# Performance work log

Hardware: AMD Instinct MI355X
Metric: run time of the kernel (lower is better)

## Reference

```python
import jax, jax.numpy as jnp
import numpy as np

B, L, S, D, H, DH = 32, 96, 96, 512, 8, 64  # d_ff = S*S = 9216


def setup_inputs() -> dict:
    key = jax.random.key(0)
    ks = jax.random.split(key, 13)
    sc = 0.02
    inp = {
        "queries": jax.random.normal(ks[0], (B, L, D), jnp.float32),
        "keys": jax.random.normal(ks[1], (B, S, D), jnp.float32),
        "values": jax.random.normal(ks[2], (B, S, D), jnp.float32),
        "attn_mask": jnp.zeros((B, L, S), dtype=bool),
        # projections stored as (in, out); torch Linear is x @ W.T + b
        "Wq": jax.random.normal(ks[3], (D, H * DH), jnp.float32) * sc,
        "bq": jnp.zeros((H * DH,), jnp.float32),
        "Wk": jax.random.normal(ks[4], (D, H * DH), jnp.float32) * sc,
        "bk": jnp.zeros((H * DH,), jnp.float32),
        "Wv": jax.random.normal(ks[5], (D, H * DH), jnp.float32) * sc,
        "bv": jnp.zeros((H * DH,), jnp.float32),
        # core_value initialized as softmax over rank dim, as in the module
        "core": jax.nn.softmax(jax.random.normal(ks[6], (H, DH), jnp.float32), axis=-1),
        "Wo": jax.random.normal(ks[7], (S * S, D), jnp.float32) * sc,
        "bo": jnp.zeros((D,), jnp.float32),
    }
    return inp


def reference(queries, keys, values, attn_mask, Wq, bq, Wk, bk, Wv, bv, core, Wo, bo):
    b, l, _ = queries.shape
    s = keys.shape[1]
    h, d = core.shape
    # NOTE: the original uses .view(H, B, L, -1) on a (B, L, H*d) tensor —
    # a raw reshape, NOT a transpose. Replicate faithfully.
    q = (queries @ Wq + bq).reshape(h, b, l, d)
    k = (keys @ Wk + bk).reshape(h, b, s, d)
    v = (values @ Wv + bv).reshape(h, b, s, d)
    # per-head rank-d CP contraction, summed over heads, averaged by 1/H
    full = jnp.einsum("nh,nbih,nbjh,nbkh->bijk", core, q, k, v) / h  # [B,L,S,S]
    full = full.reshape(b, l, s * s)
    out = full @ Wo + bo  # [B, L, D]
    return out
```

## Files before the change

kernel.cpp:

```cpp
#include <hip/hip_runtime.h>
#include <hip/hip_bf16.h>
#include <stdint.h>

using bf16 = __hip_bfloat16;
typedef float v4f __attribute__((ext_vector_type(4)));
typedef short short8 __attribute__((ext_vector_type(8)));


__device__ __forceinline__ void async_cp16(void* l, const void* g) {
  __builtin_amdgcn_global_load_lds(
      (const __attribute__((address_space(1))) void*)(uintptr_t)g,
      (__attribute__((address_space(3))) void*)(uintptr_t)l, 16, 0, 0);
}

__global__ __launch_bounds__(256) void prep(
    const float* __restrict__ Wo, const float* __restrict__ Wq,
    const float* __restrict__ Wk, const float* __restrict__ Wv,
    const float* __restrict__ Xq, const float* __restrict__ Xk,
    const float* __restrict__ Xv, const float* __restrict__ bo,
    bf16* __restrict__ WoT, bf16* __restrict__ WTq,
    bf16* __restrict__ WTk, bf16* __restrict__ WTv,
    bf16* __restrict__ Xbq, bf16* __restrict__ Xbk, bf16* __restrict__ Xbv,
    float* __restrict__ out) {
  const int bid = blockIdx.x, t = threadIdx.x;
  if (bid < 5376) {
    __shared__ bf16 T[32][33];
    const float* src; bf16* dst; int K, N, kx, ny;
    if (bid < 4608) {
      src = Wo; dst = WoT; K = 9216; N = 512; kx = bid % 288; ny = bid / 288;
    } else {
      const int r = bid - 4608, which = r >> 8, rr = r & 255;
      kx = rr & 15; ny = rr >> 4; K = 512; N = 512;
      src = which == 0 ? Wq : (which == 1 ? Wk : Wv);
      dst = which == 0 ? WTq : (which == 1 ? WTk : WTv);
    }
    const int k0 = kx * 32, n0 = ny * 32;
    const int r = t >> 3, c = (t & 7) * 4;
    float4 v = *reinterpret_cast<const float4*>(src + (size_t)(k0 + r) * N + n0 + c);
    T[c + 0][r] = __float2bfloat16(v.x);
    T[c + 1][r] = __float2bfloat16(v.y);
    T[c + 2][r] = __float2bfloat16(v.z);
    T[c + 3][r] = __float2bfloat16(v.w);
    __syncthreads();
    union { uint2 u; bf16 h[4]; } o;
    o.h[0] = T[r][c + 0]; o.h[1] = T[r][c + 1];
    o.h[2] = T[r][c + 2]; o.h[3] = T[r][c + 3];
    *reinterpret_cast<uint2*>(dst + (size_t)(n0 + r) * K + k0 + c) = o.u;
  } else if (bid < 6528) {
    const int r = bid - 5376;
    const int which = r / 384, blk = r % 384;
    const float* src = which == 0 ? Xq : (which == 1 ? Xk : Xv);
    bf16* dst = which == 0 ? Xbq : (which == 1 ? Xbk : Xbv);
    const int base = blk * 4096 + t * 16;
    float4 a = *reinterpret_cast<const float4*>(src + base);
    float4 b = *reinterpret_cast<const float4*>(src + base + 4);
    float4 c = *reinterpret_cast<const float4*>(src + base + 8);
    float4 d = *reinterpret_cast<const float4*>(src + base + 12);
    union { uint4 u; bf16 h[8]; } o1, o2;
    o1.h[0] = __float2bfloat16(a.x); o1.h[1] = __float2bfloat16(a.y);
    o1.h[2] = __float2bfloat16(a.z); o1.h[3] = __float2bfloat16(a.w);
    o1.h[4] = __float2bfloat16(b.x); o1.h[5] = __float2bfloat16(b.y);
    o1.h[6] = __float2bfloat16(b.z); o1.h[7] = __float2bfloat16(b.w);
    o2.h[0] = __float2bfloat16(c.x); o2.h[1] = __float2bfloat16(c.y);
    o2.h[2] = __float2bfloat16(c.z); o2.h[3] = __float2bfloat16(c.w);
    o2.h[4] = __float2bfloat16(d.x); o2.h[5] = __float2bfloat16(d.y);
    o2.h[6] = __float2bfloat16(d.z); o2.h[7] = __float2bfloat16(d.w);
    *reinterpret_cast<uint4*>(dst + base) = o1.u;
    *reinterpret_cast<uint4*>(dst + base + 8) = o2.u;
  } else {
    const int r = bid - 6528;
    const int idx = (r * 256 + t) * 4;
    *reinterpret_cast<float4*>(out + idx) =
        *reinterpret_cast<const float4*>(bo + (idx & 511));
  }
}

__global__ __launch_bounds__(256) void proj_mfma(
    const bf16* __restrict__ Xb0, const bf16* __restrict__ Xb1,
    const bf16* __restrict__ Xb2,
    const bf16* __restrict__ WT0, const bf16* __restrict__ WT1,
    const bf16* __restrict__ WT2,
    const float* __restrict__ b0, const float* __restrict__ b1,
    const float* __restrict__ b2, const float* __restrict__ core,
    bf16* __restrict__ O0, bf16* __restrict__ O1, bf16* __restrict__ O2) {
  const int z = blockIdx.z;
  const bf16* X    = z == 0 ? Xb0 : (z == 1 ? Xb1 : Xb2);
  const bf16* WT   = z == 0 ? WT0 : (z == 1 ? WT1 : WT2);
  const float* bia = z == 0 ? b0 : (z == 1 ? b1 : b2);
  bf16* O          = z == 0 ? O0 : (z == 1 ? O1 : O2);

  const int bm = blockIdx.x * 128, bn = blockIdx.y * 64;
  __shared__ __align__(16) bf16 As[128 * 128];
  __shared__ __align__(16) bf16 Bs[64 * 128];
  const int t = threadIdx.x;
  const int w = t >> 6, lane = t & 63;
  const int m16 = lane & 15, q = lane >> 4;
  const int l16 = lane >> 4, l15 = lane & 15;

  v4f acc[2][4] = {};

  for (int k0 = 0; k0 < 512; k0 += 128) {
    __syncthreads();
    #pragma unroll
    for (int c = 0; c < 8; c++) {
      const int row = (w * 8 + c) * 4 + l16;
      const int lch = l15 ^ (row & 7);
      async_cp16(&As[(w * 8 + c) * 512],
                 X + (size_t)(bm + row) * 512 + k0 + lch * 8);
    }
    #pragma unroll
    for (int c = 0; c < 4; c++) {
      const int row = (w * 4 + c) * 4 + l16;
      const int lch = l15 ^ (row & 7);
      async_cp16(&Bs[(w * 4 + c) * 512],
                 WT + (size_t)(bn + row) * 512 + k0 + lch * 8);
    }
    __syncthreads();

    #pragma unroll
    for (int s = 0; s < 4; s++) {
      const int pc = ((s * 4 + q) ^ (m16 & 7)) * 8;
      short8 af[2], bfr[4];
      #pragma unroll
      for (int mt = 0; mt < 2; mt++)
        af[mt] = *reinterpret_cast<const short8*>(
            &As[(w * 32 + mt * 16 + m16) * 128 + pc]);
      #pragma unroll
      for (int nt = 0; nt < 4; nt++)
        bfr[nt] = *reinterpret_cast<const short8*>(
            &Bs[(nt * 16 + m16) * 128 + pc]);
      #pragma unroll
      for (int mt = 0; mt < 2; mt++)
        #pragma unroll
        for (int nt = 0; nt < 4; nt++)
          acc[mt][nt] = __builtin_amdgcn_mfma_f32_16x16x32_bf16(
              af[mt], bfr[nt], acc[mt][nt], 0, 0, 0);
    }
  }

  const bool isQ = (z == 0);
  const int nblk = bm / 384;
  #pragma unroll
  for (int mt = 0; mt < 2; mt++)
    #pragma unroll
    for (int nt = 0; nt < 4; nt++)
      #pragma unroll
      for (int r = 0; r < 4; r++) {
        const int row = bm + w * 32 + mt * 16 + q * 4 + r;
        const int col = bn + nt * 16 + m16;
        float v = acc[mt][nt][r] + bia[col];
        if (isQ) v *= core[nblk * 64 + (col & 63)] * 0.125f;
        O[(size_t)row * 512 + col] = __float2bfloat16(v);
      }
}

__global__ __launch_bounds__(256) void stage_b_mfma(
    const bf16* __restrict__ AQ, const bf16* __restrict__ KPb,
    const bf16* __restrict__ VPb, bf16* __restrict__ FULL) {
  const int b = blockIdx.y;
  const int i0 = blockIdx.x * 2;

  __shared__ __align__(16) bf16 smem[19456];
  bf16* Ks0 = smem;
  bf16* Ks1 = smem + 6144;
  bf16* Vs  = smem + 12288;
  bf16* aqs = smem + 18432;

  const int t = threadIdx.x;
  const int w = t >> 6, lane = t & 63;
  const int wr = w >> 1, wc = w & 1;
  const int m16 = lane & 15, q = lane >> 4;
  const int l8 = lane >> 3, l7 = lane & 7;

  if (t < 128) {
    const int isel = t & 1, n = t >> 4, seg = (t >> 1) & 7;
    *reinterpret_cast<uint4*>(&aqs[isel * 512 + n * 64 + seg * 8]) =
        *reinterpret_cast<const uint4*>(
            AQ + (size_t)n * 196608 + b * 6144 + (i0 + isel) * 64 + seg * 8);
  }

  union U8 { uint4 u; bf16 h[8]; };
  const int colq = (t & 7) * 8;
  const int rowk = t >> 3;
  const int krow7 = rowk & 7;

  U8 kk[3];
  {
    const bf16* Kp = KPb + b * 6144;
    #pragma unroll
    for (int c3 = 0; c3 < 3; c3++)
      kk[c3].u = *reinterpret_cast<const uint4*>(Kp + (t + c3 * 256) * 8);
  }

  v4f acc[2][3][3] = {};

  for (int n = 0; n < 8; n++) {
    __syncthreads();
    const bf16* Vp = VPb + (size_t)n * 196608 + b * 6144;
    #pragma unroll
    for (int c = 0; c < 3; c++) {
      const int r0 = (w * 3 + c) * 8;
      async_cp16(&Vs[(w * 3 + c) * 512],
                 Vp + (r0 + l8) * 64 + (l7 ^ l8) * 8);
    }
    float a0f[8], a1f[8];
    {
      U8 a0, a1;
      a0.u = *reinterpret_cast<const uint4*>(&aqs[n * 64 + colq]);
      a1.u = *reinterpret_cast<const uint4*>(&aqs[512 + n * 64 + colq]);
      #pragma unroll
      for (int e = 0; e < 8; e++) {
        a0f[e] = __bfloat162float(a0.h[e]);
        a1f[e] = __bfloat162float(a1.h[e]);
      }
    }
    #pragma unroll
    for (int c3 = 0; c3 < 3; c3++) {
      U8 s0, s1;
      #pragma unroll
      for (int e = 0; e < 8; e++) {
        const float kv = __bfloat162float(kk[c3].h[e]);
        s0.h[e] = __float2bfloat16(kv * a0f[e]);
        s1.h[e] = __float2bfloat16(kv * a1f[e]);
      }
      const int phys = (rowk + 32 * c3) * 64 + (l7 ^ krow7) * 8;
      *reinterpret_cast<uint4*>(&Ks0[phys]) = s0.u;
      *reinterpret_cast<uint4*>(&Ks1[phys]) = s1.u;
    }
    __syncthreads();
    if (n < 7) {
      const bf16* Kp1 = KPb + (size_t)(n + 1) * 196608 + b * 6144;
      #pragma unroll
      for (int c3 = 0; c3 < 3; c3++)
        kk[c3].u = *reinterpret_cast<const uint4*>(Kp1 + (t + c3 * 256) * 8);
    }

    #pragma unroll
    for (int s = 0; s < 2; s++) {
      const int pc = ((s * 4 + q) ^ (m16 & 7)) * 8;
      short8 bfr[3], af0[3], af1[3];
      #pragma unroll
      for (int cc = 0; cc < 3; cc++)
        bfr[cc] = *reinterpret_cast<const short8*>(
            &Vs[(wc * 48 + cc * 16 + m16) * 64 + pc]);
      #pragma unroll
      for (int a = 0; a < 3; a++) {
        af0[a] = *reinterpret_cast<const short8*>(
            &Ks0[(wr * 48 + a * 16 + m16) * 64 + pc]);
        af1[a] = *reinterpret_cast<const short8*>(
            &Ks1[(wr * 48 + a * 16 + m16) * 64 + pc]);
      }
      #pragma unroll
      for (int a = 0; a < 3; a++)
        #pragma unroll
        for (int cc = 0; cc < 3; cc++) {
          acc[0][a][cc] = __builtin_amdgcn_mfma_f32_16x16x32_bf16(
              af0[a], bfr[cc], acc[0][a][cc], 0, 0, 0);
          acc[1][a][cc] = __builtin_amdgcn_mfma_f32_16x16x32_bf16(
              af1[a], bfr[cc], acc[1][a][cc], 0, 0, 0);
        }
    }
  }

  __syncthreads();
  #pragma unroll
  for (int isel = 0; isel < 2; isel++)
    #pragma unroll
    for (int a = 0; a < 3; a++)
      #pragma unroll
      for (int cc = 0; cc < 3; cc++) {
        const int j0 = wr * 48 + a * 16, k0c = wc * 48 + cc * 16;
        #pragma unroll
        for (int r = 0; r < 4; r++)
          smem[isel * 9216 + (j0 + q * 4 + r) * 96 + k0c + m16] =
              __float2bfloat16(acc[isel][a][cc][r]);
      }
  __syncthreads();
  const size_t obase = (size_t)(b * 96 + i0) * 9216;
  #pragma unroll
  for (int c = t; c < 2304; c += 256)
    *reinterpret_cast<uint4*>(FULL + obase + c * 8) =
        *reinterpret_cast<const uint4*>(&smem[c * 8]);
}

__global__ __launch_bounds__(256) void stage_c_mfma(
    const bf16* __restrict__ FULL, const bf16* __restrict__ WoT,
    float* __restrict__ out) {
  const int bm = blockIdx.x * 128, bn = blockIdx.y * 64;
  const int kbase = blockIdx.z * 2304;
  __shared__ __align__(16) bf16 As[128 * 128];
  __shared__ __align__(16) bf16 Bs[64 * 128];
  const int t = threadIdx.x;
  const int w = t >> 6, lane = t & 63;
  const int m16 = lane & 15, q = lane >> 4;
  const int l16 = lane >> 4, l15 = lane & 15;

  v4f acc[2][4] = {};

  for (int k0 = kbase; k0 < kbase + 2304; k0 += 128) {
    __syncthreads();
    #pragma unroll
    for (int c = 0; c < 8; c++) {
      const int row = (w * 8 + c) * 4 + l16;
      const int lch = l15 ^ (row & 7);
      async_cp16(&As[(w * 8 + c) * 512],
                 FULL + (size_t)(bm + row) * 9216 + k0 + lch * 8);
    }
    #pragma unroll
    for (int c = 0; c < 4; c++) {
      const int row = (w * 4 + c) * 4 + l16;
      const int lch = l15 ^ (row & 7);
      async_cp16(&Bs[(w * 4 + c) * 512],
                 WoT + (size_t)(bn + row) * 9216 + k0 + lch * 8);
    }
    __syncthreads();

    #pragma unroll
    for (int s = 0; s < 4; s++) {
      const int pc = ((s * 4 + q) ^ (m16 & 7)) * 8;
      short8 af[2], bfr[4];
      #pragma unroll
      for (int mt = 0; mt < 2; mt++)
        af[mt] = *reinterpret_cast<const short8*>(
            &As[(w * 32 + mt * 16 + m16) * 128 + pc]);
      #pragma unroll
      for (int nt = 0; nt < 4; nt++)
        bfr[nt] = *reinterpret_cast<const short8*>(
            &Bs[(nt * 16 + m16) * 128 + pc]);
      #pragma unroll
      for (int mt = 0; mt < 2; mt++)
        #pragma unroll
        for (int nt = 0; nt < 4; nt++)
          acc[mt][nt] = __builtin_amdgcn_mfma_f32_16x16x32_bf16(
              af[mt], bfr[nt], acc[mt][nt], 0, 0, 0);
    }
  }

  #pragma unroll
  for (int mt = 0; mt < 2; mt++)
    #pragma unroll
    for (int nt = 0; nt < 4; nt++)
      #pragma unroll
      for (int r = 0; r < 4; r++) {
        const int row = bm + w * 32 + mt * 16 + q * 4 + r;
        const int col = bn + nt * 16 + m16;
        atomicAdd(&out[(size_t)row * 512 + col], acc[mt][nt][r]);
      }
}

extern "C" void kernel_launch(void* const* d_in, const int* in_sizes, int n_in,
                              void* d_out, int out_size, void* d_ws, size_t ws_size,
                              hipStream_t stream) {
  const float* queries = (const float*)d_in[0];
  const float* keys    = (const float*)d_in[1];
  const float* values  = (const float*)d_in[2];
  const float* Wq   = (const float*)d_in[4];
  const float* bq   = (const float*)d_in[5];
  const float* Wk   = (const float*)d_in[6];
  const float* bk   = (const float*)d_in[7];
  const float* Wv   = (const float*)d_in[8];
  const float* bv   = (const float*)d_in[9];
  const float* core = (const float*)d_in[10];
  const float* Wo   = (const float*)d_in[11];
  const float* bo   = (const float*)d_in[12];
  float* out = (float*)d_out;

  char* ws = (char*)d_ws;
  bf16* AQb = (bf16*)(ws);
  bf16* KPb = (bf16*)(ws + 3145728);
  bf16* VPb = (bf16*)(ws + 6291456);
  bf16* WTq = (bf16*)(ws + 9437184);
  bf16* WTk = (bf16*)(ws + 9961472);
  bf16* WTv = (bf16*)(ws + 10485760);
  bf16* WoT = (bf16*)(ws + 11010048);
  bf16* FULL = (bf16*)(ws + 20447232);
  bf16* Xbq = FULL;
  bf16* Xbk = FULL + 1572864;
  bf16* Xbv = FULL + 3145728;

  const dim3 blk(256);

  prep<<<dim3(8064), blk, 0, stream>>>(
      Wo, Wq, Wk, Wv, queries, keys, values, bo,
      WoT, WTq, WTk, WTv, Xbq, Xbk, Xbv, out);

  proj_mfma<<<dim3(24, 8, 3), blk, 0, stream>>>(
      Xbq, Xbk, Xbv, WTq, WTk, WTv, bq, bk, bv, core, AQb, KPb, VPb);

  stage_b_mfma<<<dim3(48, 32), blk, 0, stream>>>(AQb, KPb, VPb, FULL);

  stage_c_mfma<<<dim3(24, 8, 4), blk, 0, stream>>>(FULL, WoT, out);
}
```

Baseline: 205.4 us.

## Load A operand directly from global and halve tile rows in proj and stage_c GEMMs

Both the projection GEMM and the final Wo GEMM stop staging the A operand in LDS. Each wave now loads its A fragments straight from global memory, while B is still staged through swizzled LDS. Blocks shrink to 128 threads with 64-row tiles and the grids double to cover the same work. This is meant to cut LDS usage and barrier cost and raise occupancy, but it risks uncoalesced strided global loads for A, since each lane reads 16 bytes from a different row.

Result: slower. 236.6 us (+15.2%).

```diff
diff --git a/kernel.cpp b/kernel.cpp
--- a/kernel.cpp
+++ b/kernel.cpp
@@ -75,7 +75,7 @@
   }
 }
 
-__global__ __launch_bounds__(256) void proj_mfma(
+__global__ __launch_bounds__(128) void proj_mfma(
     const bf16* __restrict__ Xb0, const bf16* __restrict__ Xb1,
     const bf16* __restrict__ Xb2,
     const bf16* __restrict__ WT0, const bf16* __restrict__ WT1,
@@ -89,8 +89,7 @@
   const float* bia = z == 0 ? b0 : (z == 1 ? b1 : b2);
   bf16* O          = z == 0 ? O0 : (z == 1 ? O1 : O2);
 
-  const int bm = blockIdx.x * 128, bn = blockIdx.y * 64;
-  __shared__ __align__(16) bf16 As[128 * 128];
+  const int bm = blockIdx.x * 64, bn = blockIdx.y * 64;
   __shared__ __align__(16) bf16 Bs[64 * 128];
   const int t = threadIdx.x;
   const int w = t >> 6, lane = t & 63;
@@ -105,26 +104,20 @@
     for (int c = 0; c < 8; c++) {
       const int row = (w * 8 + c) * 4 + l16;
       const int lch = l15 ^ (row & 7);
-      async_cp16(&As[(w * 8 + c) * 512],
-                 X + (size_t)(bm + row) * 512 + k0 + lch * 8);
-    }
-    #pragma unroll
-    for (int c = 0; c < 4; c++) {
-      const int row = (w * 4 + c) * 4 + l16;
-      const int lch = l15 ^ (row & 7);
-      async_cp16(&Bs[(w * 4 + c) * 512],
+      async_cp16(&Bs[(w * 8 + c) * 512],
                  WT + (size_t)(bn + row) * 512 + k0 + lch * 8);
     }
     __syncthreads();
 
     #pragma unroll
     for (int s = 0; s < 4; s++) {
-      const int pc = ((s * 4 + q) ^ (m16 & 7)) * 8;
+      const int kof = k0 + s * 32 + q * 8;
       short8 af[2], bfr[4];
       #pragma unroll
       for (int mt = 0; mt < 2; mt++)
         af[mt] = *reinterpret_cast<const short8*>(
-            &As[(w * 32 + mt * 16 + m16) * 128 + pc]);
+            X + (size_t)(bm + w * 32 + mt * 16 + m16) * 512 + kof);
+      const int pc = ((s * 4 + q) ^ (m16 & 7)) * 8;
       #pragma unroll
       for (int nt = 0; nt < 4; nt++)
         bfr[nt] = *reinterpret_cast<const short8*>(
@@ -283,12 +276,11 @@
         *reinterpret_cast<const uint4*>(&smem[c * 8]);
 }
 
-__global__ __launch_bounds__(256) void stage_c_mfma(
+__global__ __launch_bounds__(128) void stage_c_mfma(
     const bf16* __restrict__ FULL, const bf16* __restrict__ WoT,
     float* __restrict__ out) {
-  const int bm = blockIdx.x * 128, bn = blockIdx.y * 64;
+  const int bm = blockIdx.x * 64, bn = blockIdx.y * 64;
   const int kbase = blockIdx.z * 2304;
-  __shared__ __align__(16) bf16 As[128 * 128];
   __shared__ __align__(16) bf16 Bs[64 * 128];
   const int t = threadIdx.x;
   const int w = t >> 6, lane = t & 63;
@@ -303,26 +295,20 @@
     for (int c = 0; c < 8; c++) {
       const int row = (w * 8 + c) * 4 + l16;
       const int lch = l15 ^ (row & 7);
-      async_cp16(&As[(w * 8 + c) * 512],
-                 FULL + (size_t)(bm + row) * 9216 + k0 + lch * 8);
-    }
-    #pragma unroll
-    for (int c = 0; c < 4; c++) {
-      const int row = (w * 4 + c) * 4 + l16;
-      const int lch = l15 ^ (row & 7);
-      async_cp16(&Bs[(w * 4 + c) * 512],
+      async_cp16(&Bs[(w * 8 + c) * 512],
                  WoT + (size_t)(bn + row) * 9216 + k0 + lch * 8);
     }
     __syncthreads();
 
     #pragma unroll
     for (int s = 0; s < 4; s++) {
-      const int pc = ((s * 4 + q) ^ (m16 & 7)) * 8;
+      const int kof = k0 + s * 32 + q * 8;
       short8 af[2], bfr[4];
       #pragma unroll
       for (int mt = 0; mt < 2; mt++)
         af[mt] = *reinterpret_cast<const short8*>(
-            &As[(w * 32 + mt * 16 + m16) * 128 + pc]);
+            FULL + (size_t)(bm + w * 32 + mt * 16 + m16) * 9216 + kof);
+      const int pc = ((s * 4 + q) ^ (m16 & 7)) * 8;
       #pragma unroll
       for (int nt = 0; nt < 4; nt++)
         bfr[nt] = *reinterpret_cast<const short8*>(
@@ -378,16 +364,14 @@
   bf16* Xbk = FULL + 1572864;
   bf16* Xbv = FULL + 3145728;
 
-  const dim3 blk(256);
-
-  prep<<<dim3(8064), blk, 0, stream>>>(
+  prep<<<dim3(8064), dim3(256), 0, stream>>>(
       Wo, Wq, Wk, Wv, queries, keys, values, bo,
       WoT, WTq, WTk, WTv, Xbq, Xbk, Xbv, out);
 
-  proj_mfma<<<dim3(24, 8, 3), blk, 0, stream>>>(
+  proj_mfma<<<dim3(48, 8, 3), dim3(128), 0, stream>>>(
       Xbq, Xbk, Xbv, WTq, WTk, WTv, bq, bk, bv, core, AQb, KPb, VPb);
 
-  stage_b_mfma<<<dim3(48, 32), blk, 0, stream>>>(AQb, KPb, VPb, FULL);
-
-  stage_c_mfma<<<dim3(24, 8, 4), blk, 0, stream>>>(FULL, WoT, out);
-}
+  stage_b_mfma<<<dim3(48, 32), dim3(256), 0, stream>>>(AQb, KPb, VPb, FULL);
+
+  stage_c_mfma<<<dim3(48, 8, 4), dim3(128), 0, stream>>>(FULL, WoT, out);
+}
```

## Double-buffer LDS tiles in output GEMM to overlap loads with MFMA

Applied to the files above, without the earlier changes.

Splits the stage C K-loop into 64-wide tiles held in two LDS buffers, issuing async global-to-LDS loads for the next tile while MFMAs consume the current one. This is meant to hide global load latency that was previously exposed between the two barriers of each iteration. Total LDS use stays the same, but tiles are smaller, so there are more barriers per K range and the swizzle pattern is adjusted for 64-element rows.

Result: no change. 202.6 us (-1.3%).

```diff
diff --git a/kernel.cpp b/kernel.cpp
--- a/kernel.cpp
+++ b/kernel.cpp
@@ -288,52 +288,64 @@
     float* __restrict__ out) {
   const int bm = blockIdx.x * 128, bn = blockIdx.y * 64;
   const int kbase = blockIdx.z * 2304;
-  __shared__ __align__(16) bf16 As[128 * 128];
-  __shared__ __align__(16) bf16 Bs[64 * 128];
+  __shared__ __align__(16) bf16 As[2][128 * 64];
+  __shared__ __align__(16) bf16 Bs[2][64 * 64];
   const int t = threadIdx.x;
   const int w = t >> 6, lane = t & 63;
   const int m16 = lane & 15, q = lane >> 4;
-  const int l16 = lane >> 4, l15 = lane & 15;
+  const int l8 = lane >> 3, l7 = lane & 7;
 
   v4f acc[2][4] = {};
 
-  for (int k0 = kbase; k0 < kbase + 2304; k0 += 128) {
-    __syncthreads();
-    #pragma unroll
-    for (int c = 0; c < 8; c++) {
-      const int row = (w * 8 + c) * 4 + l16;
-      const int lch = l15 ^ (row & 7);
-      async_cp16(&As[(w * 8 + c) * 512],
-                 FULL + (size_t)(bm + row) * 9216 + k0 + lch * 8);
-    }
-    #pragma unroll
-    for (int c = 0; c < 4; c++) {
-      const int row = (w * 4 + c) * 4 + l16;
-      const int lch = l15 ^ (row & 7);
-      async_cp16(&Bs[(w * 4 + c) * 512],
-                 WoT + (size_t)(bn + row) * 9216 + k0 + lch * 8);
-    }
-    __syncthreads();
-
-    #pragma unroll
-    for (int s = 0; s < 4; s++) {
-      const int pc = ((s * 4 + q) ^ (m16 & 7)) * 8;
-      short8 af[2], bfr[4];
-      #pragma unroll
-      for (int mt = 0; mt < 2; mt++)
-        af[mt] = *reinterpret_cast<const short8*>(
-            &As[(w * 32 + mt * 16 + m16) * 128 + pc]);
-      #pragma unroll
-      for (int nt = 0; nt < 4; nt++)
-        bfr[nt] = *reinterpret_cast<const short8*>(
-            &Bs[(nt * 16 + m16) * 128 + pc]);
-      #pragma unroll
-      for (int mt = 0; mt < 2; mt++)
-        #pragma unroll
-        for (int nt = 0; nt < 4; nt++)
-          acc[mt][nt] = __builtin_amdgcn_mfma_f32_16x16x32_bf16(
-              af[mt], bfr[nt], acc[mt][nt], 0, 0, 0);
-    }
+#define SC_STAGE(buf, k0)                                                    \
+  {                                                                          \
+    _Pragma("unroll")                                                        \
+    for (int c = 0; c < 4; c++) {                                            \
+      const int r0 = (w * 4 + c) * 8;                                        \
+      async_cp16(&As[buf][(w * 4 + c) * 512],                                \
+                 FULL + (size_t)(bm + r0 + l8) * 9216 + (k0) + (l7 ^ l8) * 8); \
+    }                                                                        \
+    _Pragma("unroll")                                                        \
+    for (int c = 0; c < 2; c++) {                                            \
+      const int r0 = (w * 2 + c) * 8;                                        \
+      async_cp16(&Bs[buf][(w * 2 + c) * 512],                                \
+                 WoT + (size_t)(bn + r0 + l8) * 9216 + (k0) + (l7 ^ l8) * 8);  \
+    }                                                                        \
+  }
+
+#define SC_COMPUTE(buf)                                                      \
+  {                                                                          \
+    _Pragma("unroll")                                                        \
+    for (int s = 0; s < 2; s++) {                                            \
+      const int pc = ((s * 4 + q) ^ (m16 & 7)) * 8;                          \
+      short8 af[2], bfr[4];                                                  \
+      _Pragma("unroll")                                                      \
+      for (int mt = 0; mt < 2; mt++)                                         \
+        af[mt] = *reinterpret_cast<const short8*>(                           \
+            &As[buf][(w * 32 + mt * 16 + m16) * 64 + pc]);                   \
+      _Pragma("unroll")                                                      \
+      for (int nt = 0; nt < 4; nt++)                                         \
+        bfr[nt] = *reinterpret_cast<const short8*>(                          \
+            &Bs[buf][(nt * 16 + m16) * 64 + pc]);                            \
+      _Pragma("unroll")                                                      \
+      for (int mt = 0; mt < 2; mt++)                                         \
+        _Pragma("unroll")                                                    \
+        for (int nt = 0; nt < 4; nt++)                                       \
+          acc[mt][nt] = __builtin_amdgcn_mfma_f32_16x16x32_bf16(             \
+              af[mt], bfr[nt], acc[mt][nt], 0, 0, 0);                        \
+    }                                                                        \
+  }
+
+  SC_STAGE(0, kbase);
+  __syncthreads();
+
+  for (int it = 0; it < 18; it++) {
+    SC_STAGE(1, kbase + (2 * it + 1) * 64);
+    SC_COMPUTE(0);
+    __syncthreads();
+    if (it < 17) SC_STAGE(0, kbase + (2 * it + 2) * 64);
+    SC_COMPUTE(1);
+    __syncthreads();
   }
 
   #pragma unroll
@@ -346,6 +358,8 @@
         const int col = bn + nt * 16 + m16;
         atomicAdd(&out[(size_t)row * 512 + col], acc[mt][nt][r]);
       }
+#undef SC_STAGE
+#undef SC_COMPUTE
 }
 
 extern "C" void kernel_launch(void* const* d_in, const int* in_sizes, int n_in,
@@ -378,16 +392,14 @@
   bf16* Xbk = FULL + 1572864;
   bf16* Xbv = FULL + 3145728;
 
-  const dim3 blk(256);
-
-  prep<<<dim3(8064), blk, 0, stream>>>(
+  prep<<<dim3(8064), dim3(256), 0, stream>>>(
       Wo, Wq, Wk, Wv, queries, keys, values, bo,
       WoT, WTq, WTk, WTv, Xbq, Xbk, Xbv, out);
 
-  proj_mfma<<<dim3(24, 8, 3), blk, 0, stream>>>(
+  proj_mfma<<<dim3(24, 8, 3), dim3(256), 0, stream>>>(
       Xbq, Xbk, Xbv, WTq, WTk, WTv, bq, bk, bv, core, AQb, KPb, VPb);
 
-  stage_b_mfma<<<dim3(48, 32), blk, 0, stream>>>(AQb, KPb, VPb, FULL);
-
-  stage_c_mfma<<<dim3(24, 8, 4), blk, 0, stream>>>(FULL, WoT, out);
-}
+  stage_b_mfma<<<dim3(48, 32), dim3(256), 0, stream>>>(AQb, KPb, VPb, FULL);
+
+  stage_c_mfma<<<dim3(24, 8, 4), dim3(256), 0, stream>>>(FULL, WoT, out);
+}
```
